# Performance work log

Hardware: AMD Instinct MI355X
Metric: run time of the kernel (lower is better)

The kernel has to match this reference:

```python
import jax, jax.numpy as jnp
import numpy as np

N = 100000   # nodes
E = 600000   # edges
F = 128      # input features
H = 128      # hidden size
A = 64       # n_actions
G = 64       # number of graphs in batch
L = 3        # GAT layers
EPS = 1e-5   # GraphNorm eps


def setup_inputs() -> dict:
    key = jax.random.key(0)
    ks = jax.random.split(key, 8)
    x = jax.random.normal(ks[0], (N, F), dtype=jnp.float32)
    edge_index = jax.random.randint(ks[1], (2, E), 0, N, dtype=jnp.int64)
    batch = jnp.sort(jax.random.randint(ks[2], (N,), 0, G, dtype=jnp.int64))
    Ws = jax.random.normal(ks[3], (L, H, H), dtype=jnp.float32) * (1.0 / np.sqrt(H))
    att_src = jax.random.normal(ks[4], (L, H), dtype=jnp.float32) * 0.1
    att_dst = jax.random.normal(ks[5], (L, H), dtype=jnp.float32) * 0.1
    conv_bias = jnp.zeros((L, H), dtype=jnp.float32)
    gn_weight = jnp.ones((L - 1, H), dtype=jnp.float32)
    gn_bias = jnp.zeros((L - 1, H), dtype=jnp.float32)
    gn_mean_scale = jnp.ones((L - 1, H), dtype=jnp.float32)
    W1 = jax.random.normal(ks[6], (H, H), dtype=jnp.float32) * (1.0 / np.sqrt(H))
    b1 = jnp.zeros((H,), dtype=jnp.float32)
    W2 = jax.random.normal(ks[7], (H, A), dtype=jnp.float32) * (1.0 / np.sqrt(H))
    b2 = jnp.zeros((A,), dtype=jnp.float32)
    return dict(x=x, edge_index=edge_index, batch=batch, Ws=Ws, att_src=att_src,
                att_dst=att_dst, conv_bias=conv_bias, gn_weight=gn_weight,
                gn_bias=gn_bias, gn_mean_scale=gn_mean_scale,
                W1=W1, b1=b1, W2=W2, b2=b2)


def reference(x, edge_index, batch, Ws, att_src, att_dst, conv_bias,
              gn_weight, gn_bias, gn_mean_scale, W1, b1, W2, b2):
    src, dst = edge_index[0], edge_index[1]
    n = x.shape[0]
    h = x
    for l in range(L):
        # GATConv (heads=1, add_self_loops=False): h' = W h, edge attention
        hW = h @ Ws[l]                              # [N,H]
        a_s = hW @ att_src[l]                       # [N]
        a_d = hW @ att_dst[l]                       # [N]
        e = jax.nn.leaky_relu(a_s[src] + a_d[dst], 0.2)      # [E]
        m = jax.ops.segment_max(e, dst, num_segments=n)      # stable softmax per dst
        ex = jnp.exp(e - m[dst])
        s = jax.ops.segment_sum(ex, dst, num_segments=n)
        alpha = ex / (s[dst] + 1e-16)               # PyG softmax eps
        h = jax.ops.segment_sum(hW[src] * alpha[:, None], dst, num_segments=n) + conv_bias[l]
        if l < L - 1:
            # GraphNorm with batch=None (source passes no batch to gnn): one graph
            mean = h.mean(axis=0, keepdims=True)
            out = h - mean * gn_mean_scale[l]
            var = (out * out).mean(axis=0, keepdims=True)
            h = gn_weight[l] * out / jnp.sqrt(var + EPS) + gn_bias[l]
            h = jax.nn.leaky_relu(h, 0.01)          # act between layers (not after last)
    pooled = jax.ops.segment_sum(h, batch, num_segments=G)   # global_add_pool [G,H]
    z = jax.nn.leaky_relu(pooled @ W1 + b1, 0.01)
    return z @ W2 + b2                               # [G,A]
```

## Files before the change

### kernel.cpp

```cpp
#include <hip/hip_runtime.h>
#include <math.h>

#define HD 128
#define GG 64
#define CSB 256
#define PSL 8

typedef __attribute__((ext_vector_type(8))) short short8;
typedef __attribute__((ext_vector_type(4))) float f32x4;
typedef __attribute__((ext_vector_type(2))) float f32x2;

__device__ __forceinline__ float leaky(float x, float s) { return x > 0.f ? x : s * x; }

__device__ __forceinline__ unsigned short bf16_of(float f) {
    union { float f; unsigned u; } v; v.f = f;
    unsigned r = v.u + 0x7fffu + ((v.u >> 16) & 1u);
    return (unsigned short)(r >> 16);
}
__device__ __forceinline__ float f_of_bf16(unsigned short u) {
    union { unsigned u; float f; } v; v.u = ((unsigned)u) << 16;
    return v.f;
}

__device__ __forceinline__ int sw(int row, int chunk) {
    return row * 128 + ((chunk ^ (row & 15)) << 3);
}

__global__ void k_init(const float* __restrict__ Ws, unsigned short* __restrict__ Wt,
                       int* __restrict__ bcnt, float* __restrict__ part,
                       float* __restrict__ pooled) {
    int i = blockIdx.x * 256 + threadIdx.x;
    if (i < 3 * 16384) {
        int l = i >> 14, rem = i & 16383;
        int nn = rem >> 7, k = rem & 127;
        Wt[i] = bf16_of(Ws[l * 16384 + k * 128 + nn]);
    }
    if (i < 513) bcnt[i] = 0;
    if (i < 2 * CSB * 256) part[i] = 0.f;
    if (i < PSL * GG * HD) pooled[i] = 0.f;
}


__global__ __launch_bounds__(256) void k_gemm_a32(
    const float* __restrict__ A, const unsigned short* __restrict__ Wt,
    const float* __restrict__ att_s, const float* __restrict__ att_d,
    unsigned short* __restrict__ hWb, float* __restrict__ a_s, float* __restrict__ a_d,
    int n) {
    __shared__ unsigned short Bs[128 * 128];
    const int tid = threadIdx.x;
    const int base = blockIdx.x * 64;

    const uint4* Wt4 = (const uint4*)Wt;
    uint4* Bs4 = (uint4*)Bs;
#pragma unroll
    for (int j = 0; j < 8; ++j) {
        int flat = tid + j * 256;
        int col = flat >> 4, c8 = flat & 15;
        Bs4[(col << 4) + (c8 ^ (col & 15))] = Wt4[flat];
    }

    const int wave = tid >> 6, lane = tid & 63;
    const int m16 = lane & 15, quad = lane >> 4;

    short8 af[4];
    {
        int row = base + wave * 16 + m16;
        row = (row < n) ? row : (n - 1);
        const float4* ap = (const float4*)(A + (size_t)row * 128);
#pragma unroll
        for (int kk = 0; kk < 4; ++kk) {
            float4 v0 = ap[kk * 8 + quad * 2];
            float4 v1 = ap[kk * 8 + quad * 2 + 1];
            union { short8 s; unsigned u[4]; } P;
            P.u[0] = (unsigned)bf16_of(v0.x) | ((unsigned)bf16_of(v0.y) << 16);
            P.u[1] = (unsigned)bf16_of(v0.z) | ((unsigned)bf16_of(v0.w) << 16);
            P.u[2] = (unsigned)bf16_of(v1.x) | ((unsigned)bf16_of(v1.y) << 16);
            P.u[3] = (unsigned)bf16_of(v1.z) | ((unsigned)bf16_of(v1.w) << 16);
            af[kk] = P.s;
        }
    }
    __syncthreads();

    f32x4 acc[8];
#pragma unroll
    for (int ct = 0; ct < 8; ++ct) acc[ct] = (f32x4){0.f, 0.f, 0.f, 0.f};
#pragma unroll
    for (int kk = 0; kk < 4; ++kk) {
#pragma unroll
        for (int ct = 0; ct < 8; ++ct) {
            short8 bfr = *(const short8*)&Bs[sw(ct * 16 + m16, kk * 4 + quad)];
            acc[ct] = __builtin_amdgcn_mfma_f32_16x16x32_bf16(af[kk], bfr, acc[ct], 0, 0, 0);
        }
    }

#pragma unroll
    for (int reg = 0; reg < 4; ++reg) {
        int gr = base + wave * 16 + quad * 4 + reg;
        bool ok = gr < n;
        unsigned short* rowp = hWb + (size_t)gr * 128 + m16;
        float s = 0.f, dd = 0.f;
#pragma unroll
        for (int ct = 0; ct < 8; ++ct) {
            float v = acc[ct][reg];
            int col = ct * 16 + m16;
            if (ok) rowp[ct * 16] = bf16_of(v);
            s = fmaf(v, att_s[col], s);
            dd = fmaf(v, att_d[col], dd);
        }
#pragma unroll
        for (int off = 1; off < 16; off <<= 1) {
            s += __shfl_xor(s, off, 64);
            dd += __shfl_xor(dd, off, 64);
        }
        if (m16 == 0 && ok) { a_s[gr] = s; a_d[gr] = dd; }
    }
}

__global__ __launch_bounds__(256) void k_gemm_a16(
    const unsigned short* __restrict__ Ab, const unsigned short* __restrict__ Wt,
    const float* __restrict__ att_s, const float* __restrict__ att_d,
    const float* __restrict__ alpha, const float* __restrict__ beta,
    unsigned short* __restrict__ hWb, float* __restrict__ a_s, float* __restrict__ a_d,
    int n) {
    __shared__ unsigned short Bs[128 * 128];
    const int tid = threadIdx.x;
    const int base = blockIdx.x * 64;

    const uint4* Wt4 = (const uint4*)Wt;
    uint4* Bs4 = (uint4*)Bs;
#pragma unroll
    for (int j = 0; j < 8; ++j) {
        int flat = tid + j * 256;
        int col = flat >> 4, c8 = flat & 15;
        Bs4[(col << 4) + (c8 ^ (col & 15))] = Wt4[flat];
    }

    const int wave = tid >> 6, lane = tid & 63;
    const int m16 = lane & 15, quad = lane >> 4;
    const float4* al4 = (const float4*)alpha;
    const float4* be4 = (const float4*)beta;

    short8 af[4];
    {
        int row = base + wave * 16 + m16;
        row = (row < n) ? row : (n - 1);
        const uint4* ap = (const uint4*)(Ab + (size_t)row * 128);
#pragma unroll
        for (int kk = 0; kk < 4; ++kk) {
            uint4 raw = ap[kk * 4 + quad];
            int c4 = kk * 8 + quad * 2;
            float4 a0 = al4[c4], a1 = al4[c4 + 1];
            float4 b0 = be4[c4], b1 = be4[c4 + 1];
            float f0 = leaky(fmaf(f_of_bf16(raw.x & 0xffff), a0.x, b0.x), 0.01f);
            float f1 = leaky(fmaf(f_of_bf16(raw.x >> 16),    a0.y, b0.y), 0.01f);
            float f2 = leaky(fmaf(f_of_bf16(raw.y & 0xffff), a0.z, b0.z), 0.01f);
            float f3 = leaky(fmaf(f_of_bf16(raw.y >> 16),    a0.w, b0.w), 0.01f);
            float f4 = leaky(fmaf(f_of_bf16(raw.z & 0xffff), a1.x, b1.x), 0.01f);
            float f5 = leaky(fmaf(f_of_bf16(raw.z >> 16),    a1.y, b1.y), 0.01f);
            float f6 = leaky(fmaf(f_of_bf16(raw.w & 0xffff), a1.z, b1.z), 0.01f);
            float f7 = leaky(fmaf(f_of_bf16(raw.w >> 16),    a1.w, b1.w), 0.01f);
            union { short8 s; unsigned u[4]; } P;
            P.u[0] = (unsigned)bf16_of(f0) | ((unsigned)bf16_of(f1) << 16);
            P.u[1] = (unsigned)bf16_of(f2) | ((unsigned)bf16_of(f3) << 16);
            P.u[2] = (unsigned)bf16_of(f4) | ((unsigned)bf16_of(f5) << 16);
            P.u[3] = (unsigned)bf16_of(f6) | ((unsigned)bf16_of(f7) << 16);
            af[kk] = P.s;
        }
    }
    __syncthreads();

    f32x4 acc[8];
#pragma unroll
    for (int ct = 0; ct < 8; ++ct) acc[ct] = (f32x4){0.f, 0.f, 0.f, 0.f};
#pragma unroll
    for (int kk = 0; kk < 4; ++kk) {
#pragma unroll
        for (int ct = 0; ct < 8; ++ct) {
            short8 bfr = *(const short8*)&Bs[sw(ct * 16 + m16, kk * 4 + quad)];
            acc[ct] = __builtin_amdgcn_mfma_f32_16x16x32_bf16(af[kk], bfr, acc[ct], 0, 0, 0);
        }
    }

#pragma unroll
    for (int reg = 0; reg < 4; ++reg) {
        int gr = base + wave * 16 + quad * 4 + reg;
        bool ok = gr < n;
        unsigned short* rowp = hWb + (size_t)gr * 128 + m16;
        float s = 0.f, dd = 0.f;
#pragma unroll
        for (int ct = 0; ct < 8; ++ct) {
            float v = acc[ct][reg];
            int col = ct * 16 + m16;
            if (ok) rowp[ct * 16] = bf16_of(v);
            s = fmaf(v, att_s[col], s);
            dd = fmaf(v, att_d[col], dd);
        }
#pragma unroll
        for (int off = 1; off < 16; off <<= 1) {
            s += __shfl_xor(s, off, 64);
            dd += __shfl_xor(dd, off, 64);
        }
        if (m16 == 0 && ok) { a_s[gr] = s; a_d[gr] = dd; }
    }
}


__global__ __launch_bounds__(256) void k_bcount(const int* __restrict__ dst,
                                                int* __restrict__ bcnt, int e) {
    __shared__ int lh[512];
    const int tid = threadIdx.x;
    for (int t = tid; t < 512; t += 256) lh[t] = 0;
    __syncthreads();
    for (int i = blockIdx.x * 256 + tid; i < e; i += gridDim.x * 256)
        atomicAdd(&lh[dst[i] >> 9], 1);
    __syncthreads();
    for (int t = tid; t < 512; t += 256)
        if (lh[t]) atomicAdd(&bcnt[t], lh[t]);
}

__global__ void k_bscan(const int* __restrict__ bcnt, int* __restrict__ bbase,
                        int* __restrict__ bcur, int* __restrict__ offs,
                        int nbk, int n, int e) {
    __shared__ int s[512];
    int t = threadIdx.x;
    int v = (t < nbk) ? bcnt[t] : 0;
    s[t] = v;
    __syncthreads();
    for (int off = 1; off < 512; off <<= 1) {
        int u = (t >= off) ? s[t - off] : 0;
        __syncthreads();
        s[t] += u;
        __syncthreads();
    }
    if (t < nbk) { bbase[t] = s[t] - v; bcur[t] = s[t] - v; }
    if (t == 0) { bbase[nbk] = e; offs[n] = e; }
}

__global__ __launch_bounds__(256) void k_part(const int* __restrict__ src,
                                              const int* __restrict__ dst,
                                              int* __restrict__ bcur,
                                              int* __restrict__ ebuf, int e) {
    __shared__ int lh[512];
    __shared__ int lbase[512];
    const int tid = threadIdx.x;
    const int chunk = (e + gridDim.x - 1) / gridDim.x;
    const int i0 = blockIdx.x * chunk;
    const int i1 = min(e, i0 + chunk);
    for (int t = tid; t < 512; t += 256) lh[t] = 0;
    __syncthreads();
    for (int i = i0 + tid; i < i1; i += 256) atomicAdd(&lh[dst[i] >> 9], 1);
    __syncthreads();
    for (int t = tid; t < 512; t += 256) {
        int c = lh[t];
        lbase[t] = c ? atomicAdd(&bcur[t], c) : 0;
    }
    __syncthreads();
    for (int t = tid; t < 512; t += 256) lh[t] = 0;
    __syncthreads();
    for (int i = i0 + tid; i < i1; i += 256) {
        int d = dst[i];
        int b = d >> 9;
        int p = lbase[b] + atomicAdd(&lh[b], 1);
        ebuf[p] = ((d & 511) << 18) | src[i];
    }
}

__global__ __launch_bounds__(256) void k_bscatter(const int* __restrict__ ebuf,
                                                  const int* __restrict__ bbase,
                                                  int* __restrict__ offs,
                                                  int* __restrict__ esrc, int n) {
    const int b = blockIdx.x;
    const int tid = threadIdx.x;
    const int nb0 = b << 9;
    const int e0 = bbase[b], e1 = bbase[b + 1];
    __shared__ int cnt[512];
    __shared__ int sc[512];
    __shared__ int pos[512];
    for (int t = tid; t < 512; t += 256) cnt[t] = 0;
    __syncthreads();
    for (int i = e0 + tid; i < e1; i += 256) atomicAdd(&cnt[ebuf[i] >> 18], 1);
    __syncthreads();
    for (int t = tid; t < 512; t += 256) sc[t] = cnt[t];
    __syncthreads();
    for (int off = 1; off < 512; off <<= 1) {
        int t0 = tid, t1 = tid + 256;
        int v0 = (t0 >= off) ? sc[t0 - off] : 0;
        int v1 = sc[t1 - off];
        __syncthreads();
        sc[t0] += v0;
        sc[t1] += v1;
        __syncthreads();
    }
    for (int t = tid; t < 512; t += 256) pos[t] = e0 + sc[t] - cnt[t];
    __syncthreads();
    for (int t = tid; t < 512; t += 256) {
        int node = nb0 + t;
        if (node < n) offs[node] = pos[t];
    }
    __syncthreads();
    for (int i = e0 + tid; i < e1; i += 256) {
        int v = ebuf[i];
        int l = v >> 18;
        int p = atomicAdd(&pos[l], 1);
        esrc[p] = v & 0x3FFFF;
    }
}

__global__ __launch_bounds__(256) void k_agg(
    const unsigned short* __restrict__ hWb,
    const int* __restrict__ offs, const int* __restrict__ esrc,
    const float* __restrict__ a_s, const float* __restrict__ a_d,
    const float* __restrict__ bias, unsigned short* __restrict__ hb,
    float* __restrict__ part, const int* __restrict__ batch,
    float* __restrict__ pooled, int n) {
    __shared__ float ss[256][9];
    __shared__ float sq[256][9];
    const int tid = threadIdx.x;
    const int l16 = tid & 15;
    const int d = blockIdx.x * 16 + (tid >> 4);
    const bool active = d < n;

    f32x2 acc0 = {0.f, 0.f}, acc1 = {0.f, 0.f}, acc2 = {0.f, 0.f}, acc3 = {0.f, 0.f};
    float ssum = 0.f;
    float h0 = 0.f, h1 = 0.f, h2 = 0.f, h3 = 0.f, h4 = 0.f, h5 = 0.f, h6 = 0.f, h7 = 0.f;

    if (active) {
        const int p0 = offs[d], p1 = offs[d + 1];
        const float ad = a_d[d];
        const uint4* hW8 = (const uint4*)hWb;

        int s_cur = (p0 < p1) ? esrc[p0] : 0;
        uint4 raw = hW8[(size_t)s_cur * 16 + l16];
        float as_cur = a_s[s_cur];
        for (int p = p0; p < p1; ++p) {
            const uint4 r = raw;
            const float e = leaky(as_cur + ad, 0.2f);
            const int pn = (p + 1 < p1) ? p + 1 : p;
            const int s_nxt = esrc[pn];
            raw = hW8[(size_t)s_nxt * 16 + l16];
            as_cur = a_s[s_nxt];

            const float ex = __expf(e);
            ssum += ex;
            const f32x2 exv = {ex, ex};
            f32x2 v;
            v.x = f_of_bf16(r.x & 0xffff); v.y = f_of_bf16(r.x >> 16);
            acc0 = __builtin_elementwise_fma(exv, v, acc0);
            v.x = f_of_bf16(r.y & 0xffff); v.y = f_of_bf16(r.y >> 16);
            acc1 = __builtin_elementwise_fma(exv, v, acc1);
            v.x = f_of_bf16(r.z & 0xffff); v.y = f_of_bf16(r.z >> 16);
            acc2 = __builtin_elementwise_fma(exv, v, acc2);
            v.x = f_of_bf16(r.w & 0xffff); v.y = f_of_bf16(r.w >> 16);
            acc3 = __builtin_elementwise_fma(exv, v, acc3);
        }

        const float inv = 1.f / (ssum + 1e-16f);
        const float4* b4p = (const float4*)bias;
        const float4 bb0 = b4p[l16 * 2], bb1 = b4p[l16 * 2 + 1];
        h0 = fmaf(acc0.x, inv, bb0.x); h1 = fmaf(acc0.y, inv, bb0.y);
        h2 = fmaf(acc1.x, inv, bb0.z); h3 = fmaf(acc1.y, inv, bb0.w);
        h4 = fmaf(acc2.x, inv, bb1.x); h5 = fmaf(acc2.y, inv, bb1.y);
        h6 = fmaf(acc3.x, inv, bb1.z); h7 = fmaf(acc3.y, inv, bb1.w);
        if (part != nullptr) {
            uint4 o;
            o.x = (unsigned)bf16_of(h0) | ((unsigned)bf16_of(h1) << 16);
            o.y = (unsigned)bf16_of(h2) | ((unsigned)bf16_of(h3) << 16);
            o.z = (unsigned)bf16_of(h4) | ((unsigned)bf16_of(h5) << 16);
            o.w = (unsigned)bf16_of(h6) | ((unsigned)bf16_of(h7) << 16);
            ((uint4*)hb)[(size_t)d * 16 + l16] = o;
        }
    }

    if (part != nullptr) {
        ss[tid][0] = active ? h0 : 0.f; sq[tid][0] = active ? h0 * h0 : 0.f;
        ss[tid][1] = active ? h1 : 0.f; sq[tid][1] = active ? h1 * h1 : 0.f;
        ss[tid][2] = active ? h2 : 0.f; sq[tid][2] = active ? h2 * h2 : 0.f;
        ss[tid][3] = active ? h3 : 0.f; sq[tid][3] = active ? h3 * h3 : 0.f;
        ss[tid][4] = active ? h4 : 0.f; sq[tid][4] = active ? h4 * h4 : 0.f;
        ss[tid][5] = active ? h5 : 0.f; sq[tid][5] = active ? h5 * h5 : 0.f;
        ss[tid][6] = active ? h6 : 0.f; sq[tid][6] = active ? h6 * h6 : 0.f;
        ss[tid][7] = active ? h7 : 0.f; sq[tid][7] = active ? h7 * h7 : 0.f;
        __syncthreads();
        if (tid < 128) {
            int c = tid >> 3, k = tid & 7;
            float S = 0.f, Q = 0.f;
#pragma unroll
            for (int g = 0; g < 16; ++g) {
                S += ss[g * 16 + c][k];
                Q += sq[g * 16 + c][k];
            }
            float* pslot = part + (size_t)(blockIdx.x & (CSB - 1)) * 256;
            atomicAdd(&pslot[tid], S);
            atomicAdd(&pslot[128 + tid], Q);
        }
    } else if (pooled != nullptr) {
        const int nb0 = blockIdx.x * 16;
        const int g0 = batch[nb0 < n ? nb0 : (n - 1)];
        const int g1 = batch[(nb0 + 15) < n ? (nb0 + 15) : (n - 1)];
        const bool isg0 = active && (batch[d] == g0);
        const bool isg1 = active && !isg0;
        ss[tid][0] = isg0 ? h0 : 0.f; sq[tid][0] = isg1 ? h0 : 0.f;
        ss[tid][1] = isg0 ? h1 : 0.f; sq[tid][1] = isg1 ? h1 : 0.f;
        ss[tid][2] = isg0 ? h2 : 0.f; sq[tid][2] = isg1 ? h2 : 0.f;
        ss[tid][3] = isg0 ? h3 : 0.f; sq[tid][3] = isg1 ? h3 : 0.f;
        ss[tid][4] = isg0 ? h4 : 0.f; sq[tid][4] = isg1 ? h4 : 0.f;
        ss[tid][5] = isg0 ? h5 : 0.f; sq[tid][5] = isg1 ? h5 : 0.f;
        ss[tid][6] = isg0 ? h6 : 0.f; sq[tid][6] = isg1 ? h6 : 0.f;
        ss[tid][7] = isg0 ? h7 : 0.f; sq[tid][7] = isg1 ? h7 : 0.f;
        __syncthreads();
        if (tid < 128) {
            int c = tid >> 3, k = tid & 7;
            float S = 0.f, Q = 0.f;
#pragma unroll
            for (int g = 0; g < 16; ++g) {
                S += ss[g * 16 + c][k];
                Q += sq[g * 16 + c][k];
            }
            float* slot = pooled + (size_t)(blockIdx.x & (PSL - 1)) * (GG * HD);
            atomicAdd(&slot[g0 * HD + tid], S);
            if (g1 != g0) atomicAdd(&slot[g1 * HD + tid], Q);
        }
    }
}

__global__ __launch_bounds__(256) void k_colfin(const float* __restrict__ part,
                                                const float* __restrict__ w,
                                                const float* __restrict__ bb,
                                                const float* __restrict__ ms,
                                                float* __restrict__ alpha,
                                                float* __restrict__ beta, float inv_n) {
    int tid = threadIdx.x;
    float a0 = 0.f, a1 = 0.f, a2 = 0.f, a3 = 0.f;
    for (int b = 0; b < CSB; b += 4) {
        a0 += part[(b + 0) * 256 + tid];
        a1 += part[(b + 1) * 256 + tid];
        a2 += part[(b + 2) * 256 + tid];
        a3 += part[(b + 3) * 256 + tid];
    }
    __shared__ float fin[256];
    fin[tid] = (a0 + a1) + (a2 + a3);
    __syncthreads();
    if (tid < 128) {
        float mean = fin[tid] * inv_n;
        float ex2 = fin[128 + tid] * inv_n;
        float m2 = mean * ms[tid];
        float var = ex2 - 2.f * m2 * mean + m2 * m2;
        float a = w[tid] * rsqrtf(var + 1e-5f);
        alpha[tid] = a;
        beta[tid] = bb[tid] - m2 * a;
    }
}

__global__ __launch_bounds__(128) void k_mlp(const float* __restrict__ pooled,
                                             const float* __restrict__ W1,
                                             const float* __restrict__ b1,
                                             const float* __restrict__ W2,
                                             const float* __restrict__ b2,
                                             float* __restrict__ out) {
    __shared__ float pr[HD];
    __shared__ float zs[HD];
    int g = blockIdx.x, t = threadIdx.x;
    float pv = 0.f;
#pragma unroll
    for (int k = 0; k < PSL; ++k) pv += pooled[(k * GG + g) * HD + t];
    pr[t] = pv;
    __syncthreads();
    float acc = b1[t];
#pragma unroll 8
    for (int k = 0; k < HD; ++k) acc = fmaf(pr[k], W1[k * HD + t], acc);
    zs[t] = leaky(acc, 0.01f);
    __syncthreads();
    if (t < 64) {
        float a2 = b2[t];
#pragma unroll 8
        for (int k = 0; k < HD; ++k) a2 = fmaf(zs[k], W2[k * 64 + t], a2);
        out[g * 64 + t] = a2;
    }
}

extern "C" void kernel_launch(void* const* d_in, const int* in_sizes, int n_in,
                              void* d_out, int out_size, void* d_ws, size_t ws_size,
                              hipStream_t stream) {
    const float* x        = (const float*)d_in[0];
    const int*   ei       = (const int*)d_in[1];
    const int*   batch    = (const int*)d_in[2];
    const float* Ws       = (const float*)d_in[3];
    const float* att_src  = (const float*)d_in[4];
    const float* att_dst  = (const float*)d_in[5];
    const float* conv_bias= (const float*)d_in[6];
    const float* gn_w     = (const float*)d_in[7];
    const float* gn_b     = (const float*)d_in[8];
    const float* gn_ms    = (const float*)d_in[9];
    const float* W1       = (const float*)d_in[10];
    const float* b1       = (const float*)d_in[11];
    const float* W2       = (const float*)d_in[12];
    const float* b2       = (const float*)d_in[13];
    float* out = (float*)d_out;

    const int n = in_sizes[2];
    const int e = in_sizes[1] / 2;
    const int* src = ei;
    const int* dst = ei + e;
    const int nbk = (n + 511) >> 9;

    char* ws = (char*)d_ws;
    unsigned short* hWb = (unsigned short*)ws;
    unsigned short* hb  = hWb + (size_t)n * HD;
    float* a_s    = (float*)(hb + (size_t)n * HD);
    float* a_d    = a_s + n;
    float* alpha  = a_d + n;
    float* beta   = alpha + HD;
    float* pooled = beta + HD;
    float* part   = pooled + PSL * GG * HD;
    unsigned short* Wt = (unsigned short*)(part + 2 * CSB * 256);
    int* offs     = (int*)(Wt + 3 * 16384);
    int* esrc     = offs + n + 1;
    int* ebuf     = esrc + e;
    int* bcnt     = ebuf + e;
    int* bbase    = bcnt + 513;
    int* bcur     = bbase + 514;

    float* part0 = part;
    float* part1 = part + CSB * 256;

    k_init<<<768, 256, 0, stream>>>(Ws, Wt, bcnt, part, pooled);
    k_bcount<<<256, 256, 0, stream>>>(dst, bcnt, e);
    k_bscan<<<1, 512, 0, stream>>>(bcnt, bbase, bcur, offs, nbk, n, e);
    k_part<<<256, 256, 0, stream>>>(src, dst, bcur, ebuf, e);
    k_bscatter<<<nbk, 256, 0, stream>>>(ebuf, bbase, offs, esrc, n);

    for (int l = 0; l < 3; ++l) {
        if (l == 0) {
            k_gemm_a32<<<(n + 63) / 64, 256, 0, stream>>>(
                x, Wt, att_src, att_dst, hWb, a_s, a_d, n);
        } else {
            k_gemm_a16<<<(n + 63) / 64, 256, 0, stream>>>(
                hb, Wt + l * 16384, att_src + l * HD, att_dst + l * HD,
                alpha, beta, hWb, a_s, a_d, n);
        }
        if (l < 2) {
            float* lpart = (l == 0) ? part0 : part1;
            k_agg<<<(n + 15) / 16, 256, 0, stream>>>(
                hWb, offs, esrc, a_s, a_d, conv_bias + l * HD, hb,
                lpart, batch, nullptr, n);
            k_colfin<<<1, 256, 0, stream>>>(lpart, gn_w + l * HD, gn_b + l * HD,
                                            gn_ms + l * HD, alpha, beta, 1.0f / n);
        } else {
            k_agg<<<(n + 15) / 16, 256, 0, stream>>>(
                hWb, offs, esrc, a_s, a_d, conv_bias + l * HD, hb,
                nullptr, batch, pooled, n);
        }
    }

    k_mlp<<<GG, HD, 0, stream>>>(pooled, W1, b1, W2, b2, out);
}
```

Measured before the change: 334.5 us.

## Merge edge-bucket histogram into init and CSR scatter into first GEMM

The bucket histogram is folded into the init kernel: 256 extra blocks write per-block histograms, and the scan kernel sums them, so no global atomics or separate count launch are needed. The per-bucket CSR scatter now runs as extra leading blocks of the layer-0 GEMM kernel, reusing its shared memory. This cuts two kernel launches and lets the independent scatter and GEMM work overlap on the device. In exchange, the scan now does a serial 256-way sum per thread and uses a larger histogram buffer.

Measured after the change: 318.5 us. 4.8% less time.

```diff
diff --git a/kernel.cpp b/kernel.cpp
--- a/kernel.cpp
+++ b/kernel.cpp
@@ -26,29 +26,135 @@
     return row * 128 + ((chunk ^ (row & 15)) << 3);
 }
 
-__global__ void k_init(const float* __restrict__ Ws, unsigned short* __restrict__ Wt,
-                       int* __restrict__ bcnt, float* __restrict__ part,
-                       float* __restrict__ pooled) {
-    int i = blockIdx.x * 256 + threadIdx.x;
+__global__ __launch_bounds__(256) void k_initb(const float* __restrict__ Ws,
+                                               unsigned short* __restrict__ Wt,
+                                               float* __restrict__ part,
+                                               float* __restrict__ pooled,
+                                               const int* __restrict__ dst,
+                                               int* __restrict__ bhist, int e) {
+    const int tid = threadIdx.x;
+    if (blockIdx.x >= 512) {
+        __shared__ int lh[512];
+        const int bi = blockIdx.x - 512;
+        for (int t = tid; t < 512; t += 256) lh[t] = 0;
+        __syncthreads();
+        const int chunk = (e + 255) / 256;
+        const int i0 = bi * chunk;
+        const int i1 = min(e, i0 + chunk);
+        for (int i = i0 + tid; i < i1; i += 256) atomicAdd(&lh[dst[i] >> 9], 1);
+        __syncthreads();
+        for (int t = tid; t < 512; t += 256) bhist[bi * 512 + t] = lh[t];
+        return;
+    }
+    int i = blockIdx.x * 256 + tid;
     if (i < 3 * 16384) {
         int l = i >> 14, rem = i & 16383;
         int nn = rem >> 7, k = rem & 127;
         Wt[i] = bf16_of(Ws[l * 16384 + k * 128 + nn]);
     }
-    if (i < 513) bcnt[i] = 0;
     if (i < 2 * CSB * 256) part[i] = 0.f;
     if (i < PSL * GG * HD) pooled[i] = 0.f;
 }
 
 
-__global__ __launch_bounds__(256) void k_gemm_a32(
+__global__ void k_bscan(const int* __restrict__ bhist, int* __restrict__ bbase,
+                        int* __restrict__ bcur, int* __restrict__ offs,
+                        int nbk, int n, int e) {
+    __shared__ int s[512];
+    int t = threadIdx.x;
+    int v = 0;
+    if (t < nbk) {
+        for (int b = 0; b < 256; ++b) v += bhist[b * 512 + t];
+    }
+    s[t] = v;
+    __syncthreads();
+    for (int off = 1; off < 512; off <<= 1) {
+        int u = (t >= off) ? s[t - off] : 0;
+        __syncthreads();
+        s[t] += u;
+        __syncthreads();
+    }
+    if (t < nbk) { bbase[t] = s[t] - v; bcur[t] = s[t] - v; }
+    if (t == 0) { bbase[nbk] = e; offs[n] = e; }
+}
+
+__global__ __launch_bounds__(256) void k_part(const int* __restrict__ src,
+                                              const int* __restrict__ dst,
+                                              int* __restrict__ bcur,
+                                              int* __restrict__ ebuf, int e) {
+    __shared__ int lh[512];
+    __shared__ int lbase[512];
+    const int tid = threadIdx.x;
+    const int chunk = (e + gridDim.x - 1) / gridDim.x;
+    const int i0 = blockIdx.x * chunk;
+    const int i1 = min(e, i0 + chunk);
+    for (int t = tid; t < 512; t += 256) lh[t] = 0;
+    __syncthreads();
+    for (int i = i0 + tid; i < i1; i += 256) atomicAdd(&lh[dst[i] >> 9], 1);
+    __syncthreads();
+    for (int t = tid; t < 512; t += 256) {
+        int c = lh[t];
+        lbase[t] = c ? atomicAdd(&bcur[t], c) : 0;
+    }
+    __syncthreads();
+    for (int t = tid; t < 512; t += 256) lh[t] = 0;
+    __syncthreads();
+    for (int i = i0 + tid; i < i1; i += 256) {
+        int d = dst[i];
+        int b = d >> 9;
+        int p = lbase[b] + atomicAdd(&lh[b], 1);
+        ebuf[p] = ((d & 511) << 18) | src[i];
+    }
+}
+
+__global__ __launch_bounds__(256) void k_gemm_a32_bsc(
     const float* __restrict__ A, const unsigned short* __restrict__ Wt,
     const float* __restrict__ att_s, const float* __restrict__ att_d,
     unsigned short* __restrict__ hWb, float* __restrict__ a_s, float* __restrict__ a_d,
-    int n) {
+    const int* __restrict__ ebuf, const int* __restrict__ bbase,
+    int* __restrict__ offs, int* __restrict__ esrc, int nbk, int n) {
     __shared__ unsigned short Bs[128 * 128];
     const int tid = threadIdx.x;
-    const int base = blockIdx.x * 64;
+
+    if (blockIdx.x < nbk) {
+        int* cnt = (int*)Bs;
+        int* sc  = cnt + 512;
+        int* pos = sc + 512;
+        const int b = blockIdx.x;
+        const int nb0 = b << 9;
+        const int e0 = bbase[b], e1 = bbase[b + 1];
+        for (int t = tid; t < 512; t += 256) cnt[t] = 0;
+        __syncthreads();
+        for (int i = e0 + tid; i < e1; i += 256) atomicAdd(&cnt[ebuf[i] >> 18], 1);
+        __syncthreads();
+        for (int t = tid; t < 512; t += 256) sc[t] = cnt[t];
+        __syncthreads();
+        for (int off = 1; off < 512; off <<= 1) {
+            int t0 = tid, t1 = tid + 256;
+            int v0 = (t0 >= off) ? sc[t0 - off] : 0;
+            int v1 = sc[t1 - off];
+            __syncthreads();
+            sc[t0] += v0;
+            sc[t1] += v1;
+            __syncthreads();
+        }
+        for (int t = tid; t < 512; t += 256) pos[t] = e0 + sc[t] - cnt[t];
+        __syncthreads();
+        for (int t = tid; t < 512; t += 256) {
+            int node = nb0 + t;
+            if (node < n) offs[node] = pos[t];
+        }
+        __syncthreads();
+        for (int i = e0 + tid; i < e1; i += 256) {
+            int v = ebuf[i];
+            int l = v >> 18;
+            int p = atomicAdd(&pos[l], 1);
+            esrc[p] = v & 0x3FFFF;
+        }
+        return;
+    }
+
+    const int base = (blockIdx.x - nbk) * 64;
 
     const uint4* Wt4 = (const uint4*)Wt;
     uint4* Bs4 = (uint4*)Bs;
@@ -204,108 +310,6 @@
     }
 }
 
-
-__global__ __launch_bounds__(256) void k_bcount(const int* __restrict__ dst,
-                                                int* __restrict__ bcnt, int e) {
-    __shared__ int lh[512];
-    const int tid = threadIdx.x;
-    for (int t = tid; t < 512; t += 256) lh[t] = 0;
-    __syncthreads();
-    for (int i = blockIdx.x * 256 + tid; i < e; i += gridDim.x * 256)
-        atomicAdd(&lh[dst[i] >> 9], 1);
-    __syncthreads();
-    for (int t = tid; t < 512; t += 256)
-        if (lh[t]) atomicAdd(&bcnt[t], lh[t]);
-}
-
-__global__ void k_bscan(const int* __restrict__ bcnt, int* __restrict__ bbase,
-                        int* __restrict__ bcur, int* __restrict__ offs,
-                        int nbk, int n, int e) {
-    __shared__ int s[512];
-    int t = threadIdx.x;
-    int v = (t < nbk) ? bcnt[t] : 0;
-    s[t] = v;
-    __syncthreads();
-    for (int off = 1; off < 512; off <<= 1) {
-        int u = (t >= off) ? s[t - off] : 0;
-        __syncthreads();
-        s[t] += u;
-        __syncthreads();
-    }
-    if (t < nbk) { bbase[t] = s[t] - v; bcur[t] = s[t] - v; }
-    if (t == 0) { bbase[nbk] = e; offs[n] = e; }
-}
-
-__global__ __launch_bounds__(256) void k_part(const int* __restrict__ src,
-                                              const int* __restrict__ dst,
-                                              int* __restrict__ bcur,
-                                              int* __restrict__ ebuf, int e) {
-    __shared__ int lh[512];
-    __shared__ int lbase[512];
-    const int tid = threadIdx.x;
-    const int chunk = (e + gridDim.x - 1) / gridDim.x;
-    const int i0 = blockIdx.x * chunk;
-    const int i1 = min(e, i0 + chunk);
-    for (int t = tid; t < 512; t += 256) lh[t] = 0;
-    __syncthreads();
-    for (int i = i0 + tid; i < i1; i += 256) atomicAdd(&lh[dst[i] >> 9], 1);
-    __syncthreads();
-    for (int t = tid; t < 512; t += 256) {
-        int c = lh[t];
-        lbase[t] = c ? atomicAdd(&bcur[t], c) : 0;
-    }
-    __syncthreads();
-    for (int t = tid; t < 512; t += 256) lh[t] = 0;
-    __syncthreads();
-    for (int i = i0 + tid; i < i1; i += 256) {
-        int d = dst[i];
-        int b = d >> 9;
-        int p = lbase[b] + atomicAdd(&lh[b], 1);
-        ebuf[p] = ((d & 511) << 18) | src[i];
-    }
-}
-
-__global__ __launch_bounds__(256) void k_bscatter(const int* __restrict__ ebuf,
-                                                  const int* __restrict__ bbase,
-                                                  int* __restrict__ offs,
-                                                  int* __restrict__ esrc, int n) {
-    const int b = blockIdx.x;
-    const int tid = threadIdx.x;
-    const int nb0 = b << 9;
-    const int e0 = bbase[b], e1 = bbase[b + 1];
-    __shared__ int cnt[512];
-    __shared__ int sc[512];
-    __shared__ int pos[512];
-    for (int t = tid; t < 512; t += 256) cnt[t] = 0;
-    __syncthreads();
-    for (int i = e0 + tid; i < e1; i += 256) atomicAdd(&cnt[ebuf[i] >> 18], 1);
-    __syncthreads();
-    for (int t = tid; t < 512; t += 256) sc[t] = cnt[t];
-    __syncthreads();
-    for (int off = 1; off < 512; off <<= 1) {
-        int t0 = tid, t1 = tid + 256;
-        int v0 = (t0 >= off) ? sc[t0 - off] : 0;
-        int v1 = sc[t1 - off];
-        __syncthreads();
-        sc[t0] += v0;
-        sc[t1] += v1;
-        __syncthreads();
-    }
-    for (int t = tid; t < 512; t += 256) pos[t] = e0 + sc[t] - cnt[t];
-    __syncthreads();
-    for (int t = tid; t < 512; t += 256) {
-        int node = nb0 + t;
-        if (node < n) offs[node] = pos[t];
-    }
-    __syncthreads();
-    for (int i = e0 + tid; i < e1; i += 256) {
-        int v = ebuf[i];
-        int l = v >> 18;
-        int p = atomicAdd(&pos[l], 1);
-        esrc[p] = v & 0x3FFFF;
-    }
-}
-
 __global__ __launch_bounds__(256) void k_agg(
     const unsigned short* __restrict__ hWb,
     const int* __restrict__ offs, const int* __restrict__ esrc,
@@ -516,24 +520,23 @@
     int* offs     = (int*)(Wt + 3 * 16384);
     int* esrc     = offs + n + 1;
     int* ebuf     = esrc + e;
-    int* bcnt     = ebuf + e;
-    int* bbase    = bcnt + 513;
+    int* bhist    = ebuf + e;
+    int* bbase    = bhist + 256 * 512;
     int* bcur     = bbase + 514;
 
     float* part0 = part;
     float* part1 = part + CSB * 256;
 
-    k_init<<<768, 256, 0, stream>>>(Ws, Wt, bcnt, part, pooled);
-    k_bcount<<<256, 256, 0, stream>>>(dst, bcnt, e);
-    k_bscan<<<1, 512, 0, stream>>>(bcnt, bbase, bcur, offs, nbk, n, e);
+    k_initb<<<768, 256, 0, stream>>>(Ws, Wt, part, pooled, dst, bhist, e);
+    k_bscan<<<1, 512, 0, stream>>>(bhist, bbase, bcur, offs, nbk, n, e);
     k_part<<<256, 256, 0, stream>>>(src, dst, bcur, ebuf, e);
-    k_bscatter<<<nbk, 256, 0, stream>>>(ebuf, bbase, offs, esrc, n);
+
+    k_gemm_a32_bsc<<<nbk + (n + 63) / 64, 256, 0, stream>>>(
+        x, Wt, att_src, att_dst, hWb, a_s, a_d,
+        ebuf, bbase, offs, esrc, nbk, n);
 
     for (int l = 0; l < 3; ++l) {
-        if (l == 0) {
-            k_gemm_a32<<<(n + 63) / 64, 256, 0, stream>>>(
-                x, Wt, att_src, att_dst, hWb, a_s, a_d, n);
-        } else {
+        if (l > 0) {
             k_gemm_a16<<<(n + 63) / 64, 256, 0, stream>>>(
                 hb, Wt + l * 16384, att_src + l * HD, att_dst + l * HD,
                 alpha, beta, hWb, a_s, a_d, n);
```
